# Kernel tuning notes

Hardware: AMD Instinct MI355X
Metric: run time of the kernel (lower is better)

## Reference

```python
import jax, jax.numpy as jnp
import numpy as np

N, E, F, C, K, N_G, N_M = 100000, 600000, 6, 128, 3, 2, 2


def setup_inputs() -> dict:
    key = jax.random.key(0)
    ks = jax.random.split(key, 12)
    x = jax.random.normal(ks[0], (N, F), dtype=jnp.float32)
    edge_index = jax.random.randint(ks[1], (2, E), 0, N, dtype=jnp.int32)
    s = 0.05
    W0 = jax.random.normal(ks[2], (F, C), dtype=jnp.float32) * s
    b0 = jnp.zeros((C,), dtype=jnp.float32)
    # TAGConv: per layer, K+1 hop weights (no per-lin bias) + one shared bias
    W_tag = jax.random.normal(ks[3], (N_G, K + 1, C, C), dtype=jnp.float32) * s
    b_tag = jnp.zeros((N_G, C), dtype=jnp.float32)
    W_mlp = jax.random.normal(ks[4], (N_M, C, C), dtype=jnp.float32) * s
    b_mlp = jnp.zeros((N_M, C), dtype=jnp.float32)
    W1 = jax.random.normal(ks[5], (C, 1), dtype=jnp.float32) * s
    b1 = jnp.zeros((1,), dtype=jnp.float32)
    return {"x": x, "edge_index": edge_index, "W0": W0, "b0": b0,
            "W_tag": W_tag, "b_tag": b_tag, "W_mlp": W_mlp, "b_mlp": b_mlp,
            "W1": W1, "b1": b1}


def reference(x, edge_index, W0, b0, W_tag, b_tag, W_mlp, b_mlp, W1, b1):
    row, col = edge_index[0], edge_index[1]  # source -> target
    n = x.shape[0]
    # GCN-style symmetric normalization, no self-loops (PyG TAGConv default)
    deg = jax.ops.segment_sum(jnp.ones((row.shape[0],), x.dtype), col, num_segments=n)
    dis = jnp.where(deg > 0, jax.lax.rsqrt(jnp.maximum(deg, 1.0)), 0.0)
    norm = dis[row] * dis[col]  # [E]

    h = jax.nn.relu(x @ W0 + b0)  # lin0

    for g in range(W_tag.shape[0]):  # n_G TAGConv layers
        out = h @ W_tag[g, 0]
        xk = h
        for k in range(1, W_tag.shape[1]):  # K hops
            msg = norm[:, None] * xk[row]           # [E, C] gather
            xk = jax.ops.segment_sum(msg, col, num_segments=n)  # scatter-add
            out = out + xk @ W_tag[g, k]
        h = jax.nn.relu(out + b_tag[g])

    for m in range(W_mlp.shape[0]):  # mlp block
        h = jax.nn.relu(h @ W_mlp[m] + b_mlp[m])

    return jax.nn.relu(h @ W1 + b1)  # [N, 1]
```

## Files before the change

kernel.cpp:

```cpp
#include <hip/hip_runtime.h>

#define NN 100000
#define NP 100096
#define NE 600000
#define CC 128

typedef __attribute__((ext_vector_type(4))) float f32x4;
typedef _Float16 h8 __attribute__((ext_vector_type(8)));
typedef _Float16 h2 __attribute__((ext_vector_type(2)));


__global__ void k_deg(const int* __restrict__ col, int* __restrict__ deg) {
  int e = blockIdx.x * 256 + threadIdx.x;
  if (e < NE) atomicAdd(&deg[col[e]], 1);
}

__global__ void k_dis(const int* __restrict__ deg, float* __restrict__ dis) {
  int n = blockIdx.x * 256 + threadIdx.x;
  if (n >= NP) return;
  int d = (n < NN) ? deg[n] : 0;
  dis[n] = (d > 0) ? rsqrtf((float)d) : 0.0f;
}

__global__ void k_scan1(const int* __restrict__ deg, int* __restrict__ rowptr,
                        int* __restrict__ bsum) {
  __shared__ int s[1024];
  int t = threadIdx.x;
  int i = blockIdx.x * 1024 + t;
  int v = (i < NN) ? deg[i] : 0;
  s[t] = v;
  __syncthreads();
  #pragma unroll
  for (int off = 1; off < 1024; off <<= 1) {
    int tv = (t >= off) ? s[t - off] : 0;
    __syncthreads();
    s[t] += tv;
    __syncthreads();
  }
  if (i < NN) rowptr[i] = s[t] - v;
  if (t == 1023) bsum[blockIdx.x] = s[1023];
}

__global__ void k_scan2(const int* __restrict__ bsum, int* __restrict__ bsum2) {
  __shared__ int s[128];
  int t = threadIdx.x;
  int v = (t < 98) ? bsum[t] : 0;
  s[t] = v;
  __syncthreads();
  #pragma unroll
  for (int off = 1; off < 128; off <<= 1) {
    int tv = (t >= off) ? s[t - off] : 0;
    __syncthreads();
    s[t] += tv;
    __syncthreads();
  }
  bsum2[t] = s[t] - v;
}

__global__ void k_scan3(int* __restrict__ rowptr, const int* __restrict__ bsum2) {
  int i = blockIdx.x * 1024 + threadIdx.x;
  if (i < NN) rowptr[i] += bsum2[blockIdx.x];
}

__global__ void k_fill(const int* __restrict__ row, const int* __restrict__ col,
                       const float* __restrict__ dis, const int* __restrict__ rowptr,
                       int* __restrict__ cnt, int2* __restrict__ csr) {
  int e = blockIdx.x * 256 + threadIdx.x;
  if (e >= NE) return;
  int c = col[e], r = row[e];
  int pos = rowptr[c] + atomicAdd(&cnt[c], 1);
  int2 v;
  v.x = r * CC;
  v.y = __float_as_int(dis[r] * dis[c]);
  csr[pos] = v;
}


__global__ void k_lin0(const float* __restrict__ x, const float* __restrict__ W0,
                       const float* __restrict__ b0, _Float16* __restrict__ h) {
  int idx = blockIdx.x * 256 + threadIdx.x;
  int n = idx >> 7, c = idx & 127;
  if (n >= NP) return;
  float v = 0.0f;
  if (n < NN) {
    v = b0[c];
    #pragma unroll
    for (int f = 0; f < 6; ++f) v = fmaf(x[n * 6 + f], W0[f * CC + c], v);
    v = fmaxf(v, 0.0f);
  }
  h[idx] = (_Float16)v;
}


__global__ void k_wconv(const float* __restrict__ src, _Float16* __restrict__ dst, int K) {
  int tid = blockIdx.x * 256 + threadIdx.x;
  if (tid >= K * 128) return;
  int e = tid & 7, l = (tid >> 3) & 63, nb = (tid >> 9) & 7, kb = tid >> 12;
  int k = kb * 32 + (l >> 4) * 8 + e;
  int c = nb * 16 + (l & 15);
  dst[tid] = (_Float16)src[k * 128 + c];
}


__global__ void k_prop(const int* __restrict__ rowptr, const int* __restrict__ deg,
                       const int2* __restrict__ csr,
                       const _Float16* __restrict__ xin, _Float16* __restrict__ xout) {
  int gid = blockIdx.x * 256 + threadIdx.x;
  int wid = gid >> 6;
  int lane = gid & 63;
  if (wid >= NP) return;
  float a0 = 0.0f, a1 = 0.0f;
  if (wid < NN) {
    int start = rowptr[wid], d = deg[wid];
    int2 ew; ew.x = 0; ew.y = 0;
    if (lane < d) ew = csr[start + lane];
    int nd = d < 64 ? d : 64;
    int nd4 = (nd + 3) & ~3;
    for (int j = 0; j < nd4; j += 4) {
      #pragma unroll
      for (int u = 0; u < 4; ++u) {
        int off = __shfl(ew.x, j + u);
        float w = __uint_as_float(__shfl(ew.y, j + u));
        h2 v = *reinterpret_cast<const h2*>(&xin[off + lane * 2]);
        a0 += w * (float)v[0];
        a1 += w * (float)v[1];
      }
    }
    if (d > 64) {
      for (int j = start + 64; j < start + d; ++j) {
        int2 e2 = csr[j];
        float w = __uint_as_float(e2.y);
        h2 v = *reinterpret_cast<const h2*>(&xin[e2.x + lane * 2]);
        a0 += w * (float)v[0];
        a1 += w * (float)v[1];
      }
    }
  }
  h2 o; o[0] = (_Float16)a0; o[1] = (_Float16)a1;
  *reinterpret_cast<h2*>(&xout[wid * CC + lane * 2]) = o;
}


template<int KB, bool BR>
__global__ __launch_bounds__(256) void k_mm(const _Float16* __restrict__ X0,
                                            const _Float16* __restrict__ X1,
                                            const _Float16* __restrict__ X2,
                                            const _Float16* __restrict__ X3,
                                            const _Float16* __restrict__ Wp,
                                            const float* __restrict__ bias,
                                            _Float16* __restrict__ Y) {
  __shared__ _Float16 lds[128 * 128];
  int t = threadIdx.x;
  int w = t >> 6, l = t & 63;
  int lr = l & 15, lk = l >> 4;
  int m0w = (w & 1) * 64;
  int nb0 = (w >> 1) * 4;
  long row0 = (long)blockIdx.x * 128;
  const _Float16* Xs[4] = {X0, X1, X2, X3};

  f32x4 acc[4][4];
  #pragma unroll
  for (int m = 0; m < 4; ++m)
    #pragma unroll
    for (int n = 0; n < 4; ++n) acc[m][n] = (f32x4){0.f, 0.f, 0.f, 0.f};

  #pragma unroll
  for (int xi = 0; xi < KB; ++xi) {
    const _Float16* __restrict__ xb = Xs[xi];
    #pragma unroll
    for (int i = 0; i < 8; ++i) {
      int li = i * 256 + t;
      int r = li >> 4, ck = li & 15;
      int cs = ck ^ (r & 7);
      const _Float16* src = xb + (size_t)(row0 + r) * CC + cs * 8;
      _Float16* dst = lds + ((size_t)i * 2048 + (size_t)(t & 192) * 8);
      __builtin_amdgcn_global_load_lds((const __attribute__((address_space(1))) void*)src,
                                       (__attribute__((address_space(3))) void*)dst,
                                       16, 0, 0);
    }
    __syncthreads();

    #pragma unroll
    for (int kk = 0; kk < 4; ++kk) {
      int kb = xi * 4 + kk;
      h8 a[4], b[4];
      #pragma unroll
      for (int m = 0; m < 4; ++m) {
        int R = m0w + m * 16 + lr;
        a[m] = *reinterpret_cast<const h8*>(&lds[R * 128 + (((kk * 4 + lk) ^ (lr & 7)) << 3)]);
      }
      #pragma unroll
      for (int n = 0; n < 4; ++n)
        b[n] = *reinterpret_cast<const h8*>(&Wp[((size_t)(kb * 8 + nb0 + n) * 64 + l) * 8]);
      #pragma unroll
      for (int m = 0; m < 4; ++m)
        #pragma unroll
        for (int n = 0; n < 4; ++n)
          acc[m][n] = __builtin_amdgcn_mfma_f32_16x16x32_f16(a[m], b[n], acc[m][n], 0, 0, 0);
    }
    __syncthreads();
  }

  int r0 = m0w + lk * 4;
  long rb = row0 + r0;
  #pragma unroll
  for (int m = 0; m < 4; ++m) {
    #pragma unroll
    for (int n = 0; n < 4; ++n) {
      int c = (nb0 + n) * 16 + lr;
      float bv = BR ? bias[c] : 0.0f;
      #pragma unroll
      for (int q = 0; q < 4; ++q) {
        float v = acc[m][n][q] + bv;
        if (BR) v = fmaxf(v, 0.0f);
        Y[(rb + m * 16 + q) * CC + c] = (_Float16)v;
      }
    }
  }
}


__global__ void k_head(const _Float16* __restrict__ h, const float* __restrict__ W1,
                       const float* __restrict__ b1, float* __restrict__ out) {
  int gid = blockIdx.x * 256 + threadIdx.x;
  int wid = gid >> 6, lane = gid & 63;
  if (wid >= NN) return;
  const _Float16* hp = &h[wid * CC];
  float v = (float)hp[lane] * W1[lane] + (float)hp[lane + 64] * W1[lane + 64];
  #pragma unroll
  for (int o = 32; o > 0; o >>= 1) v += __shfl_down(v, o);
  if (lane == 0) out[wid] = fmaxf(v + b1[0], 0.0f);
}


extern "C" void kernel_launch(void* const* d_in, const int* in_sizes, int n_in,
                              void* d_out, int out_size, void* d_ws, size_t ws_size,
                              hipStream_t stream) {
  const float* x     = (const float*)d_in[0];
  const int*   ei    = (const int*)d_in[1];
  const float* W0    = (const float*)d_in[2];
  const float* b0    = (const float*)d_in[3];
  const float* W_tag = (const float*)d_in[4];
  const float* b_tag = (const float*)d_in[5];
  const float* W_mlp = (const float*)d_in[6];
  const float* b_mlp = (const float*)d_in[7];
  const float* W1    = (const float*)d_in[8];
  const float* b1    = (const float*)d_in[9];
  const int* row = ei;
  const int* col = ei + NE;

  char* p = (char*)d_ws;
  auto carve = [&](size_t bytes) { void* r = (void*)p; p += (bytes + 255) & ~(size_t)255; return r; };
  _Float16* hA   = (_Float16*)carve((size_t)NP * CC * 2);
  _Float16* hB   = (_Float16*)carve((size_t)NP * CC * 2);
  _Float16* x1   = (_Float16*)carve((size_t)NP * CC * 2);
  _Float16* x2   = (_Float16*)carve((size_t)NP * CC * 2);
  _Float16* x3   = (_Float16*)carve((size_t)NP * CC * 2);
  _Float16* WpT0 = (_Float16*)carve((size_t)512 * CC * 2);
  _Float16* WpT1 = (_Float16*)carve((size_t)512 * CC * 2);
  _Float16* WpM0 = (_Float16*)carve((size_t)CC * CC * 2);
  _Float16* WpM1 = (_Float16*)carve((size_t)CC * CC * 2);
  float* dis     = (float*)carve((size_t)NP * 4);
  int*   deg     = (int*)carve((size_t)NP * 4);
  int*   rowptr  = (int*)carve((size_t)NN * 4);
  int*   cnt     = (int*)carve((size_t)NN * 4);
  int*   bsum    = (int*)carve(512);
  int*   bsum2   = (int*)carve(512);
  int2*  csr     = (int2*)carve((size_t)NE * 8);

  hipMemsetAsync(deg, 0, (size_t)NP * 4, stream);
  hipMemsetAsync(cnt, 0, (size_t)NN * 4, stream);

  k_deg<<<(NE + 255) / 256, 256, 0, stream>>>(col, deg);
  k_dis<<<(NP + 255) / 256, 256, 0, stream>>>(deg, dis);
  k_scan1<<<98, 1024, 0, stream>>>(deg, rowptr, bsum);
  k_scan2<<<1, 128, 0, stream>>>(bsum, bsum2);
  k_scan3<<<98, 1024, 0, stream>>>(rowptr, bsum2);
  k_fill<<<(NE + 255) / 256, 256, 0, stream>>>(row, col, dis, rowptr, cnt, csr);

  k_wconv<<<(512 * CC + 255) / 256, 256, 0, stream>>>(W_tag,            WpT0, 512);
  k_wconv<<<(512 * CC + 255) / 256, 256, 0, stream>>>(W_tag + 512 * CC, WpT1, 512);
  k_wconv<<<(CC * CC + 255) / 256, 256, 0, stream>>>(W_mlp,             WpM0, 128);
  k_wconv<<<(CC * CC + 255) / 256, 256, 0, stream>>>(W_mlp + CC * CC,   WpM1, 128);

  k_lin0<<<NP * CC / 256, 256, 0, stream>>>(x, W0, b0, hA);

  const int GB = NP / 128;
  const int PB = NP * 64 / 256;

  _Float16* hc = hA;
  _Float16* hn = hB;
  const _Float16* WpT[2] = {WpT0, WpT1};
  for (int g = 0; g < 2; ++g) {
    k_prop<<<PB, 256, 0, stream>>>(rowptr, deg, csr, hc, x1);
    k_prop<<<PB, 256, 0, stream>>>(rowptr, deg, csr, x1, x2);
    k_prop<<<PB, 256, 0, stream>>>(rowptr, deg, csr, x2, x3);
    k_mm<4, true><<<GB, 256, 0, stream>>>(hc, x1, x2, x3, WpT[g], b_tag + (size_t)g * CC, hn);
    _Float16* tmp = hc; hc = hn; hn = tmp;
  }

  k_mm<1, true><<<GB, 256, 0, stream>>>(hc, nullptr, nullptr, nullptr, WpM0, b_mlp, hn);
  { _Float16* tmp = hc; hc = hn; hn = tmp; }
  k_mm<1, true><<<GB, 256, 0, stream>>>(hc, nullptr, nullptr, nullptr, WpM1, b_mlp + CC, hn);
  { _Float16* tmp = hc; hc = hn; hn = tmp; }

  k_head<<<(NN * 64) / 256, 256, 0, stream>>>(hc, W1, b1, (float*)d_out);
}
```

Measured before the change: 411.7 us.

## Process four destination nodes per wavefront in CSR propagation kernel

The propagation kernel now has each 64-lane wavefront handle four consecutive destination nodes instead of one. It loads all of their edges in one coalesced CSR read and routes each edge's contribution to the right node through per-lane group masks and eight accumulators. The aim is to fill the wavefront better, since average degree is about 6 and one node per wave leaves most lanes' edge slots idle, and to cut per-wave setup cost. In exchange every edge now does four multiply-adds per channel pair instead of one, with more registers, and rowptr is padded up to NP+8 by a small tail kernel.

```diff
diff --git a/kernel.cpp b/kernel.cpp
--- a/kernel.cpp
+++ b/kernel.cpp
@@ -60,6 +60,11 @@
 __global__ void k_scan3(int* __restrict__ rowptr, const int* __restrict__ bsum2) {
   int i = blockIdx.x * 1024 + threadIdx.x;
   if (i < NN) rowptr[i] += bsum2[blockIdx.x];
+}
+
+__global__ void k_rptail(int* __restrict__ rowptr) {
+  int i = NN + blockIdx.x * 256 + threadIdx.x;
+  if (i < NP + 8) rowptr[i] = NE;
 }
 
 __global__ void k_fill(const int* __restrict__ row, const int* __restrict__ col,
@@ -102,42 +107,73 @@
 }
 
 
-__global__ void k_prop(const int* __restrict__ rowptr, const int* __restrict__ deg,
-                       const int2* __restrict__ csr,
-                       const _Float16* __restrict__ xin, _Float16* __restrict__ xout) {
+__global__ __launch_bounds__(256) void k_prop(const int* __restrict__ rowptr,
+                                              const int2* __restrict__ csr,
+                                              const _Float16* __restrict__ xin,
+                                              _Float16* __restrict__ xout) {
   int gid = blockIdx.x * 256 + threadIdx.x;
-  int wid = gid >> 6;
+  int wv = gid >> 6;
   int lane = gid & 63;
-  if (wid >= NP) return;
-  float a0 = 0.0f, a1 = 0.0f;
-  if (wid < NN) {
-    int start = rowptr[wid], d = deg[wid];
-    int2 ew; ew.x = 0; ew.y = 0;
-    if (lane < d) ew = csr[start + lane];
-    int nd = d < 64 ? d : 64;
-    int nd4 = (nd + 3) & ~3;
-    for (int j = 0; j < nd4; j += 4) {
-      #pragma unroll
-      for (int u = 0; u < 4; ++u) {
-        int off = __shfl(ew.x, j + u);
-        float w = __uint_as_float(__shfl(ew.y, j + u));
-        h2 v = *reinterpret_cast<const h2*>(&xin[off + lane * 2]);
-        a0 += w * (float)v[0];
-        a1 += w * (float)v[1];
-      }
+  int n0 = wv * 4;
+  if (n0 >= NP) return;
+  int b0 = rowptr[n0], b1 = rowptr[n0 + 1], b2 = rowptr[n0 + 2],
+      b3 = rowptr[n0 + 3], b4 = rowptr[n0 + 4];
+  int e4 = b4 - b0;
+
+  int2 ew; ew.x = 0; ew.y = 0;
+  int gl = 0;
+  if (lane < e4) {
+    int pos = b0 + lane;
+    ew = csr[pos];
+    gl = (pos >= b1) + (pos >= b2) + (pos >= b3);
+  }
+
+  float a00 = 0, a01 = 0, a10 = 0, a11 = 0, a20 = 0, a21 = 0, a30 = 0, a31 = 0;
+  int nb = e4 < 64 ? e4 : 64;
+  for (int j = 0; j < nb; j += 8) {
+    #pragma unroll
+    for (int u = 0; u < 8; ++u) {
+      int off = __shfl(ew.x, j + u);
+      float w = __uint_as_float(__shfl(ew.y, j + u));
+      int gg = __shfl(gl, j + u);
+      h2 v = *reinterpret_cast<const h2*>(&xin[off + lane * 2]);
+      float v0 = (float)v[0], v1 = (float)v[1];
+      float w0 = (gg == 0) ? w : 0.0f;
+      float w1 = (gg == 1) ? w : 0.0f;
+      float w2 = (gg == 2) ? w : 0.0f;
+      float w3 = (gg == 3) ? w : 0.0f;
+      a00 += w0 * v0; a01 += w0 * v1;
+      a10 += w1 * v0; a11 += w1 * v1;
+      a20 += w2 * v0; a21 += w2 * v1;
+      a30 += w3 * v0; a31 += w3 * v1;
     }
-    if (d > 64) {
-      for (int j = start + 64; j < start + d; ++j) {
-        int2 e2 = csr[j];
-        float w = __uint_as_float(e2.y);
-        h2 v = *reinterpret_cast<const h2*>(&xin[e2.x + lane * 2]);
-        a0 += w * (float)v[0];
-        a1 += w * (float)v[1];
-      }
-    }
-  }
-  h2 o; o[0] = (_Float16)a0; o[1] = (_Float16)a1;
-  *reinterpret_cast<h2*>(&xout[wid * CC + lane * 2]) = o;
+  }
+  for (int j = 64; j < e4; ++j) {
+    int pos = b0 + j;
+    int2 e2 = csr[pos];
+    float w = __uint_as_float(e2.y);
+    int gg = (pos >= b1) + (pos >= b2) + (pos >= b3);
+    h2 v = *reinterpret_cast<const h2*>(&xin[e2.x + lane * 2]);
+    float v0 = (float)v[0], v1 = (float)v[1];
+    float w0 = (gg == 0) ? w : 0.0f;
+    float w1 = (gg == 1) ? w : 0.0f;
+    float w2 = (gg == 2) ? w : 0.0f;
+    float w3 = (gg == 3) ? w : 0.0f;
+    a00 += w0 * v0; a01 += w0 * v1;
+    a10 += w1 * v0; a11 += w1 * v1;
+    a20 += w2 * v0; a21 += w2 * v1;
+    a30 += w3 * v0; a31 += w3 * v1;
+  }
+
+  h2 o;
+  o[0] = (_Float16)a00; o[1] = (_Float16)a01;
+  *reinterpret_cast<h2*>(&xout[(size_t)(n0 + 0) * CC + lane * 2]) = o;
+  o[0] = (_Float16)a10; o[1] = (_Float16)a11;
+  *reinterpret_cast<h2*>(&xout[(size_t)(n0 + 1) * CC + lane * 2]) = o;
+  o[0] = (_Float16)a20; o[1] = (_Float16)a21;
+  *reinterpret_cast<h2*>(&xout[(size_t)(n0 + 2) * CC + lane * 2]) = o;
+  o[0] = (_Float16)a30; o[1] = (_Float16)a31;
+  *reinterpret_cast<h2*>(&xout[(size_t)(n0 + 3) * CC + lane * 2]) = o;
 }
 
 
@@ -262,7 +298,7 @@
   _Float16* WpM1 = (_Float16*)carve((size_t)CC * CC * 2);
   float* dis     = (float*)carve((size_t)NP * 4);
   int*   deg     = (int*)carve((size_t)NP * 4);
-  int*   rowptr  = (int*)carve((size_t)NN * 4);
+  int*   rowptr  = (int*)carve((size_t)(NP + 8) * 4);
   int*   cnt     = (int*)carve((size_t)NN * 4);
   int*   bsum    = (int*)carve(512);
   int*   bsum2   = (int*)carve(512);
@@ -276,6 +312,7 @@
   k_scan1<<<98, 1024, 0, stream>>>(deg, rowptr, bsum);
   k_scan2<<<1, 128, 0, stream>>>(bsum, bsum2);
   k_scan3<<<98, 1024, 0, stream>>>(rowptr, bsum2);
+  k_rptail<<<1, 256, 0, stream>>>(rowptr);
   k_fill<<<(NE + 255) / 256, 256, 0, stream>>>(row, col, dis, rowptr, cnt, csr);
 
   k_wconv<<<(512 * CC + 255) / 256, 256, 0, stream>>>(W_tag,            WpT0, 512);
@@ -286,15 +323,15 @@
   k_lin0<<<NP * CC / 256, 256, 0, stream>>>(x, W0, b0, hA);
 
   const int GB = NP / 128;
-  const int PB = NP * 64 / 256;
+  const int PB = (NP / 4) * 64 / 256;
 
   _Float16* hc = hA;
   _Float16* hn = hB;
   const _Float16* WpT[2] = {WpT0, WpT1};
   for (int g = 0; g < 2; ++g) {
-    k_prop<<<PB, 256, 0, stream>>>(rowptr, deg, csr, hc, x1);
-    k_prop<<<PB, 256, 0, stream>>>(rowptr, deg, csr, x1, x2);
-    k_prop<<<PB, 256, 0, stream>>>(rowptr, deg, csr, x2, x3);
+    k_prop<<<PB, 256, 0, stream>>>(rowptr, csr, hc, x1);
+    k_prop<<<PB, 256, 0, stream>>>(rowptr, csr, x1, x2);
+    k_prop<<<PB, 256, 0, stream>>>(rowptr, csr, x2, x3);
     k_mm<4, true><<<GB, 256, 0, stream>>>(hc, x1, x2, x3, WpT[g], b_tag + (size_t)g * CC, hn);
     _Float16* tmp = hc; hc = hn; hn = tmp;
   }
```

After: 402.1 us. 1.02x faster.
